# Kernel tuning notes

Measured on AMD Instinct MI355X. Metric: run time of the kernel, lower is better.

Reference implementation:

```python
import jax, jax.numpy as jnp
import numpy as np

B, T, I, H, NL, HORIZON, NQ = 256, 512, 64, 512, 2, 30, 3
MEDIAN_IDX = 1  # quantiles.index(0.5)


def _lstm_cell(xt, h, c, Wih, Whh, b):
    # PyTorch gate order: i, f, g, o
    g = xt @ Wih.T + h @ Whh.T + b
    i, f, gg, o = jnp.split(g, 4, axis=-1)
    c_new = jax.nn.sigmoid(f) * c + jax.nn.sigmoid(i) * jnp.tanh(gg)
    h_new = jax.nn.sigmoid(o) * jnp.tanh(c_new)
    return h_new, c_new


def _run_lstm_layer(xs, Wih, Whh, b):
    # xs: [T, B, in]; zero initial state (torch default)
    batch = xs.shape[1]
    hidden = Whh.shape[1]
    h0 = jnp.zeros((batch, hidden), xs.dtype)

    def step(carry, xt):
        h, c = carry
        h, c = _lstm_cell(xt, h, c, Wih, Whh, b)
        return (h, c), h

    (hT, cT), hs = jax.lax.scan(step, (h0, h0), xs)
    return hs, hT, cT


def setup_inputs() -> dict:
    key = jax.random.key(0)
    ks = jax.random.split(key, 24)
    k = 1.0 / np.sqrt(H)

    def u(kk, shape):
        return jax.random.uniform(kk, shape, jnp.float32, -k, k)

    inp = {
        "x": jax.random.normal(ks[0], (B, T, I), jnp.float32),
        # encoder layer 0 (input I) and layer 1 (input H)
        "enc_Wih0": u(ks[1], (4 * H, I)),
        "enc_Whh0": u(ks[2], (4 * H, H)),
        "enc_bih0": u(ks[3], (4 * H,)),
        "enc_bhh0": u(ks[4], (4 * H,)),
        "enc_Wih1": u(ks[5], (4 * H, H)),
        "enc_Whh1": u(ks[6], (4 * H, H)),
        "enc_bih1": u(ks[7], (4 * H,)),
        "enc_bhh1": u(ks[8], (4 * H,)),
        # decoder layer 0 (input H+1) and layer 1 (input H)
        "dec_Wih0": u(ks[9], (4 * H, H + 1)),
        "dec_Whh0": u(ks[10], (4 * H, H)),
        "dec_bih0": u(ks[11], (4 * H,)),
        "dec_bhh0": u(ks[12], (4 * H,)),
        "dec_Wih1": u(ks[13], (4 * H, H)),
        "dec_Whh1": u(ks[14], (4 * H, H)),
        "dec_bih1": u(ks[15], (4 * H,)),
        "dec_bhh1": u(ks[16], (4 * H,)),
        # attention: W [H,H] (no bias), V [H] (Linear(H,1) weight)
        "attn_W": u(ks[17], (H, H)),
        "attn_v": u(ks[18], (H,)),
        # output projection [NQ, H] + bias
        "out_W": u(ks[19], (NQ, H)),
        "out_b": u(ks[20], (NQ,)),
    }
    return inp


def reference(x, enc_Wih0, enc_Whh0, enc_bih0, enc_bhh0,
              enc_Wih1, enc_Whh1, enc_bih1, enc_bhh1,
              dec_Wih0, dec_Whh0, dec_bih0, dec_bhh0,
              dec_Wih1, dec_Whh1, dec_bih1, dec_bhh1,
              attn_W, attn_v, out_W, out_b):
    # ---- encoder: 2-layer LSTM over time (eval mode: no dropout) ----
    xs = jnp.transpose(x, (1, 0, 2))  # [T, B, I]
    hs0, _, _ = _run_lstm_layer(xs, enc_Wih0, enc_Whh0, enc_bih0 + enc_bhh0)
    hs1, h_last, c_last = _run_lstm_layer(hs0, enc_Wih1, enc_Whh1, enc_bih1 + enc_bhh1)
    encoder_outputs = jnp.transpose(hs1, (1, 0, 2))  # [B, T, H]

    # precompute W(encoder_outputs) once (same math as per-step recompute)
    enc_proj = jnp.einsum('bth,gh->btg', encoder_outputs, attn_W)  # [B, T, H]

    b_dec0 = dec_bih0 + dec_bhh0
    b_dec1 = dec_bih1 + dec_bhh1

    dec_input0 = x[:, -1, 0:1]  # [B, 1]

    def step(carry, _):
        h, c, inp = carry
        # Bahdanau attention
        dec_proj = h @ attn_W.T  # [B, H]
        energies = jnp.einsum('bth,h->bt', jnp.tanh(enc_proj + dec_proj[:, None, :]), attn_v)
        attn = jax.nn.softmax(energies, axis=1)  # [B, T]
        ctx = jnp.einsum('bt,bth->bh', attn, encoder_outputs)  # [B, H]
        # decoder LSTM, 1 timestep; both layers restart from the SAME (h, c)
        # (the module repeats the last layer's state across layers each step)
        x0 = jnp.concatenate([inp, ctx], axis=1)  # [B, H+1]
        h0, c0 = _lstm_cell(x0, h, c, dec_Wih0, dec_Whh0, b_dec0)
        h1, c1 = _lstm_cell(h0, h, c, dec_Wih1, dec_Whh1, b_dec1)
        out = h1 @ out_W.T + out_b  # [B, NQ]
        new_inp = out[:, MEDIAN_IDX:MEDIAN_IDX + 1]  # feed back median quantile
        return (h1, c1, new_inp), out

    _, preds = jax.lax.scan(step, (h_last, c_last, dec_input0), None, length=HORIZON)
    return jnp.transpose(preds, (1, 0, 2))  # [B, HORIZON, NQ]
```

## Files before the change

### kernel.cpp

```cpp
#include <hip/hip_runtime.h>


typedef _Float16 half_t;
typedef __attribute__((ext_vector_type(8)))  _Float16 f16x8;
typedef __attribute__((ext_vector_type(16))) float    f32x16;

#define MFMA(a,b,c) __builtin_amdgcn_mfma_f32_32x32x16_f16((a),(b),(c),0,0,0)
#define CBAR()      asm volatile("" ::: "memory")

template<int N> __device__ __forceinline__ void waitvm() {
  asm volatile("s_waitcnt vmcnt(%0)" :: "n"(N) : "memory");
}

__device__ __forceinline__ float fsig(float x)  { return 1.0f / (1.0f + __expf(-x)); }
__device__ __forceinline__ float ftanh(float x) { return 1.0f - 2.0f / (1.0f + __expf(2.0f * x)); }

union FU { float f; unsigned u; };
union HU { _Float16 h; unsigned short u; };

template<bool FAST>
__device__ __forceinline__ float ldfa(const float* p) {
  if constexpr (FAST) {
    float v;
    asm volatile("global_load_dword %0, %1, off sc0\n\ts_waitcnt vmcnt(0)"
                 : "=v"(v) : "v"(p) : "memory");
    return v;
  } else {
    unsigned v = __hip_atomic_load((const unsigned*)p, __ATOMIC_RELAXED, __HIP_MEMORY_SCOPE_AGENT);
    FU c; c.u = v; return c.f;
  }
}
template<bool FAST>
__device__ __forceinline__ void stfa(float* p, float v) {
  FU c; c.f = v;
  if constexpr (FAST)
    asm volatile("global_store_dword %0, %1, off sc0" :: "v"(p), "v"(c.u) : "memory");
  else
    __hip_atomic_store((unsigned*)p, c.u, __ATOMIC_RELAXED, __HIP_MEMORY_SCOPE_AGENT);
}
template<bool FAST>
__device__ __forceinline__ void stha(half_t* p, float v) {
  HU c; c.h = (half_t)v;
  if constexpr (FAST)
    asm volatile("global_store_short %0, %1, off sc0" :: "v"(p), "v"((unsigned)c.u) : "memory");
  else
    __hip_atomic_store((unsigned short*)p, c.u, __ATOMIC_RELAXED, __HIP_MEMORY_SCOPE_AGENT);
}
template<bool FAST>
__device__ __forceinline__ void st64(float* p, float a, float b) {
  FU x, y; x.f = a; y.f = b;
  unsigned long long v = (unsigned long long)x.u | ((unsigned long long)y.u << 32);
  if constexpr (FAST)
    asm volatile("global_store_dwordx2 %0, %1, off sc0" :: "v"(p), "v"(v) : "memory");
  else
    __hip_atomic_store((unsigned long long*)p, v, __ATOMIC_RELAXED, __HIP_MEMORY_SCOPE_AGENT);
}
template<bool FAST>
__device__ __forceinline__ void ld64(const float* p, float& a, float& b) {
  unsigned long long v;
  if constexpr (FAST) {
    asm volatile("global_load_dwordx2 %0, %1, off sc0\n\ts_waitcnt vmcnt(0)"
                 : "=v"(v) : "v"(p) : "memory");
  } else {
    v = __hip_atomic_load((const unsigned long long*)p, __ATOMIC_RELAXED, __HIP_MEMORY_SCOPE_AGENT);
  }
  FU x, y; x.u = (unsigned)v; y.u = (unsigned)(v >> 32); a = x.f; b = y.f;
}

static constexpr size_t O_X16 = 0;
static constexpr size_t O_WL0 = O_X16 + (size_t)512*256*128*2;
static constexpr size_t O_WL1 = O_WL0 + (size_t)2048*640*2;
static constexpr size_t O_WP1 = O_WL1 + (size_t)2048*1024*2;
static constexpr size_t O_WD0 = O_WP1 + (size_t)4672*512*2;
static constexpr size_t O_WD1 = O_WD0 + (size_t)2048*512*2;
static constexpr size_t O_BL0 = O_WD1 + (size_t)2048*512*2;
static constexpr size_t O_BL1 = O_BL0 + 8192;
static constexpr size_t O_BD0 = O_BL1 + 8192;
static constexpr size_t O_BD1 = O_BD0 + 8192;
static constexpr size_t O_W0C = O_BD1 + 8192;
static constexpr size_t O_H0B = O_W0C + 8192;
static constexpr size_t O_H1B = O_H0B + (size_t)2*256*512*2;
static constexpr size_t O_HD1 = O_H1B + (size_t)2*256*512*2;
static constexpr size_t O_H0D = O_HD1 + (size_t)256*512*2;
static constexpr size_t O_CTX = O_H0D + (size_t)256*512*2;
static constexpr size_t O_C0  = O_CTX + (size_t)256*512*2;
static constexpr size_t O_C1  = O_C0  + (size_t)256*512*4;
static constexpr size_t O_INP = O_C1  + (size_t)256*512*4;
static constexpr size_t O_GAT = O_INP + 1024;
static constexpr size_t O_EO  = O_GAT + (size_t)256*4672*4;
static constexpr size_t O_EP  = O_EO  + (size_t)256*512*512*2;
static constexpr size_t WS_NEED = O_EP + (size_t)256*512*512*2;

__device__ __align__(4096) unsigned char g_ws[WS_NEED];
__device__ int g_bar[2048];
__device__ int g_flags[1024];
__device__ int g_xcc[256];

#define WSH(o) ((half_t*)(g_ws + (o)))
#define WSCH(o) ((const half_t*)(g_ws + (o)))
#define WSF(o) ((float*)(g_ws + (o)))
#define WSCF(o) ((const float*)(g_ws + (o)))
#define BLINE(i) (g_bar + ((size_t)(i) << 5))

__device__ __forceinline__ int gperm(int n) { return (n & 3) * 512 + (n >> 2); }

__device__ __forceinline__ void gbarf(int g, int r, int step) {
  __syncthreads();
  if (threadIdx.x < 64) {
    if (threadIdx.x == 0)
      __hip_atomic_store(&g_flags[(g << 5) + r], step,
                         __ATOMIC_RELAXED, __HIP_MEMORY_SCOPE_AGENT);
    const int* fp = &g_flags[(g << 5) + (threadIdx.x & 31)];
    for (;;) {
      int v = __hip_atomic_load(fp, __ATOMIC_RELAXED, __HIP_MEMORY_SCOPE_AGENT);
      if (__all(v >= step)) break;
      __builtin_amdgcn_s_sleep(1);
    }
  }
  __syncthreads();
}

__device__ __forceinline__ void gbar_acq8() {
  __syncthreads();
  if (threadIdx.x == 0) {
    const int g = blockIdx.x & 7;
    int* cnt = BLINE(g);
    int* mst = BLINE(8);
    int* gs  = BLINE(16 + g);
    int old = __hip_atomic_load(gs, __ATOMIC_RELAXED, __HIP_MEMORY_SCOPE_AGENT);
    int a = __hip_atomic_fetch_add(cnt, 1, __ATOMIC_ACQ_REL, __HIP_MEMORY_SCOPE_AGENT);
    if (a == 31) {
      __hip_atomic_store(cnt, 0, __ATOMIC_RELAXED, __HIP_MEMORY_SCOPE_AGENT);
      int m = __hip_atomic_fetch_add(mst, 1, __ATOMIC_ACQ_REL, __HIP_MEMORY_SCOPE_AGENT);
      if (m == 7) {
        __hip_atomic_store(mst, 0, __ATOMIC_RELAXED, __HIP_MEMORY_SCOPE_AGENT);
        for (int q = 0; q < 8; q++)
          __hip_atomic_fetch_add(BLINE(16 + q), 1, __ATOMIC_RELEASE, __HIP_MEMORY_SCOPE_AGENT);
      }
    }
    while (__hip_atomic_load(gs, __ATOMIC_RELAXED, __HIP_MEMORY_SCOPE_AGENT) == old)
      __builtin_amdgcn_s_sleep(2);
    (void)__hip_atomic_load(gs, __ATOMIC_ACQUIRE, __HIP_MEMORY_SCOPE_AGENT);
  }
  __syncthreads();
}

template<int AX>
__device__ __forceinline__ void gld(const half_t* gp, char* lp) {
  __builtin_amdgcn_global_load_lds(
      (const __attribute__((address_space(1))) unsigned int*)gp,
      (__attribute__((address_space(3))) unsigned int*)lp, 16, 0, AX);
}

struct Seg { const half_t* p; int stride; int row0; };

template<int AXA, int AXB>
__device__ __forceinline__ void stageA(Seg sa, Seg sb, int cSplit, int c,
                                       int lane, int wid, char* dst) {
  bool isA = c < cSplit;
  Seg s = isA ? sa : sb;
  int kb = (isA ? c : (c - cSplit)) * 128;
  const half_t* gp = s.p + (size_t)(s.row0 + (lane & 31)) * s.stride
                         + kb + (wid << 4) + ((lane >> 5) << 3);
  if (isA) {
    gld<AXA>(gp, dst);
    gld<AXA>(gp + (size_t)32 * s.stride, dst + 1024);
  } else {
    gld<AXB>(gp, dst);
    gld<AXB>(gp + (size_t)32 * s.stride, dst + 1024);
  }
}

template<int C, int NC>
__device__ __forceinline__ void kks(int lane, int wid, char* asg, f32x16 acc[2][2],
                                    f16x8 (&b0)[4], f16x8 (&b1)[4]) {
  if constexpr (C < NC) {
    waitvm<4 * (NC - 1 - C)>();
    char* ab = asg + (size_t)(C * 8 + wid) * 2048 + lane * 16;
    f16x8 a0 = *(const f16x8*)ab;
    f16x8 a1 = *(const f16x8*)(ab + 1024);
    acc[0][0] = MFMA(a0, b0[C], acc[0][0]);
    acc[0][1] = MFMA(a0, b1[C], acc[0][1]);
    acc[1][0] = MFMA(a1, b0[C], acc[1][0]);
    acc[1][1] = MFMA(a1, b1[C], acc[1][1]);
    CBAR();
    kks<C + 1, NC>(lane, wid, asg, acc, b0, b1);
  }
}

template<int NC, int AXA, int AXB>
__device__ __forceinline__ void gemm_ks(Seg sa, Seg sb, int cSplit, const half_t* Wt,
                                        int lane, int wid, char* asg, f32x16 acc[2][2]) {
  const half_t* wb = Wt + (wid << 1) * 512 + lane * 8;
  f16x8 b0[4], b1[4];
  #pragma unroll
  for (int c = 0; c < NC; c++) {
    stageA<AXA, AXB>(sa, sb, cSplit, c, lane, wid, asg + (size_t)(c * 8 + wid) * 2048);
    CBAR();
    b0[c] = *(const f16x8*)(wb + (size_t)c * 8192);
    b1[c] = *(const f16x8*)(wb + (size_t)c * 8192 + 512);
    CBAR();
  }
  kks<0, NC>(lane, wid, asg, acc, b0, b1);
}

template<int C, int NC>
__device__ __forceinline__ void kks32(char* wslr, f32x16 (&acc)[2][2],
                                      f16x8 (&b0)[4], f16x8 (&b1)[4]) {
  if constexpr (C < NC) {
    waitvm<3 * (NC - 1 - C) + 2>();
    f16x8 a = *(const f16x8*)(wslr + C * 8192);
    acc[0][0] = MFMA(a, b0[C], acc[0][0]);
    acc[0][1] = MFMA(a, b1[C], acc[0][1]);
    CBAR();
    kks32<C + 1, NC>(wslr, acc, b0, b1);
  }
}

template<int NC, int AX>
__device__ __forceinline__ void gemm_ks32(const half_t* aP, const half_t* Wt,
                                          int lane, int wid, char* asg, f32x16 (&acc)[2][2]) {
  char* wsl = asg + wid * 1024;
  const half_t* wb = Wt + (wid << 1) * 512 + lane * 8;
  f16x8 b0[4], b1[4];
  #pragma unroll
  for (int c = 0; c < NC; c++) {
    gld<AX>(aP + c * 128, wsl + c * 8192);
    CBAR();
    b0[c] = *(const f16x8*)(wb + (size_t)c * 8192);
    b1[c] = *(const f16x8*)(wb + (size_t)c * 8192 + 512);
    CBAR();
  }
  kks32<0, NC>(wsl + lane * 16, acc, b0, b1);
}

template<int C>
__device__ __forceinline__ void encL0(const char* wslr, const f16x8 (&B0)[5],
                                      const f16x8 (&B1)[5], f32x16 (&acc)[2][2]) {
  if constexpr (C < 5) {
    waitvm<8 - C>();
    f16x8 a = *(const f16x8*)(wslr + C * 8192);
    acc[0][0] = MFMA(a, B0[C], acc[0][0]);
    acc[0][1] = MFMA(a, B1[C], acc[0][1]);
    CBAR();
    encL0<C + 1>(wslr, B0, B1, acc);
  }
}
template<int C>
__device__ __forceinline__ void encL1(const char* wslr, const f16x8 (&B0)[8],
                                      const f16x8 (&B1)[8], f32x16 (&acc)[2][2]) {
  if constexpr (C < 8) {
    if constexpr (C >= 4) waitvm<7 - C>();
    f16x8 a = *(const f16x8*)(wslr + (C + 1) * 8192);
    acc[1][0] = MFMA(a, B0[C], acc[1][0]);
    acc[1][1] = MFMA(a, B1[C], acc[1][1]);
    CBAR();
    encL1<C + 1>(wslr, B0, B1, acc);
  }
}

__device__ __forceinline__ void acc_wr(float* dst, int lane, f32x16 acc[2][2]) {
  #pragma unroll
  for (int t = 0; t < 4; t++) {
    f32x16 a = acc[t >> 1][t & 1];
    #pragma unroll
    for (int r4 = 0; r4 < 4; r4++)
      *(float4*)(dst + ((t * 4 + r4) * 64 + lane) * 4) =
          make_float4(a[r4*4], a[r4*4+1], a[r4*4+2], a[r4*4+3]);
  }
}
__device__ __forceinline__ void acc_add(const float* src, int lane, f32x16 acc[2][2]) {
  #pragma unroll
  for (int t = 0; t < 4; t++) {
    #pragma unroll
    for (int r4 = 0; r4 < 4; r4++) {
      float4 v = *(const float4*)(src + ((t * 4 + r4) * 64 + lane) * 4);
      acc[t>>1][t&1][r4*4]   += v.x;
      acc[t>>1][t&1][r4*4+1] += v.y;
      acc[t>>1][t&1][r4*4+2] += v.z;
      acc[t>>1][t&1][r4*4+3] += v.w;
    }
  }
}
__device__ __forceinline__ void reduce8(f32x16 acc[2][2], float* red, int lane, int wid) {
  if (wid >= 4) acc_wr(red + (size_t)(wid - 4) * 4096, lane, acc);
  __syncthreads();
  if (wid < 4) acc_add(red + (size_t)wid * 4096, lane, acc);
  if (wid == 2 || wid == 3) acc_wr(red + (size_t)wid * 4096, lane, acc);
  __syncthreads();
  if (wid < 2) {
    acc_add(red + (size_t)(wid + 2) * 4096, lane, acc);
    float* zone = red + 8192 + (size_t)wid * 4096;
    #pragma unroll
    for (int ms = 0; ms < 2; ms++)
      #pragma unroll
      for (int ns = 0; ns < 2; ns++)
        #pragma unroll
        for (int rr = 0; rr < 16; rr++) {
          int row = ms * 32 + (rr & 3) + ((rr >> 2) << 3) + ((lane >> 5) << 2);
          zone[row * 64 + ns * 32 + (lane & 31)] = acc[ms][ns][rr];
        }
  }
  __syncthreads();
}
__device__ __forceinline__ float4 rsum4(const float* red, int row, int col) {
  float4 a = *(const float4*)&red[8192 + row * 64 + col];
  float4 b = *(const float4*)&red[12288 + row * 64 + col];
  return make_float4(a.x + b.x, a.y + b.y, a.z + b.z, a.w + b.w);
}

template<bool FAST>
__device__ __noinline__ void run_all(int g, int r, const float* attn_v,
                                     const float* out_b, float* out,
                                     char* asg, float* red) {
  constexpr int AXH = FAST ? 1 : 17;
  constexpr size_t PP = (size_t)256 * 512;

  const half_t* x16 = WSCH(O_X16);
  const half_t* wL0 = WSCH(O_WL0);
  const half_t* wL1 = WSCH(O_WL1);
  const half_t* wP1 = WSCH(O_WP1);
  const half_t* wD0 = WSCH(O_WD0);
  const half_t* wD1 = WSCH(O_WD1);
  half_t* h0bB = WSH(O_H0B);
  half_t* h1bB = WSH(O_H1B);
  half_t* hd1  = WSH(O_HD1);
  half_t* h0d  = WSH(O_H0D);
  half_t* ctx  = WSH(O_CTX);
  half_t* eo   = WSH(O_EO);
  half_t* ep   = WSH(O_EP);
  float* c1 = WSF(O_C1);
  float* inp = WSF(O_INP);
  float* gates = WSF(O_GAT);

  const int tid = threadIdx.x;
  const int wid = tid >> 6;
  const int lane = tid & 63;
  const int m0 = g << 5;
  const f32x16 zv = {0,0,0,0,0,0,0,0,0,0,0,0,0,0,0,0};
  int bstep = 0;

  const int koff = (wid << 4) + ((lane >> 5) << 3);
  const size_t aofs = (size_t)(m0 + (lane & 31)) * 512 + koff;
  const size_t xofs = (size_t)(m0 + (lane & 31)) * 128 + koff;
  char* wsl = asg + wid * 1024;
  const char* wslr = wsl + lane * 16;

  {
    const int n0 = r << 6;
    const half_t* wb0 = wL0 + (size_t)r * (5 * 8192) + (wid << 1) * 512 + lane * 8;
    const half_t* wb1 = wL1 + (size_t)r * (8 * 8192) + (wid << 1) * 512 + lane * 8;
    f16x8 B0L0[5], B1L0[5], B0L1[8], B1L1[8];
    #pragma unroll
    for (int c = 0; c < 5; c++) {
      B0L0[c] = *(const f16x8*)(wb0 + (size_t)c * 8192);
      B1L0[c] = *(const f16x8*)(wb0 + (size_t)c * 8192 + 512);
    }
    #pragma unroll
    for (int c = 0; c < 8; c++) {
      B0L1[c] = *(const f16x8*)(wb1 + (size_t)c * 8192);
      B1L1[c] = *(const f16x8*)(wb1 + (size_t)c * 8192 + 512);
    }
    const int eu = tid & 15, ebl = tid >> 4;
    const float4 breg0 = *(const float4*)&(WSCF(O_BL0))[n0 + eu * 4];
    const float4 breg1 = *(const float4*)&(WSCF(O_BL1))[n0 + eu * 4];
    const int bg = m0 + ebl, ug = (r << 4) + eu;
    float creg0 = 0.f, creg1 = 0.f;

    for (int s = 0; s <= 512; s++) {
      {
        const int tc = s < 512 ? s : 511;
        const half_t* xp  = x16 + (((size_t)tc) << 15) + xofs;
        const half_t* h0p = h0bB + (size_t)((s + 1) & 1) * PP + aofs;
        const half_t* h1p = h1bB + (size_t)(s & 1) * PP + aofs;
        gld<0>(xp, wsl);
        #pragma unroll
        for (int c = 0; c < 4; c++) gld<AXH>(h0p + c * 128, wsl + (c + 1) * 8192);
        #pragma unroll
        for (int c = 0; c < 4; c++) gld<AXH>(h1p + c * 128, wsl + (c + 5) * 8192);
        CBAR();
      }
      f32x16 acc[2][2] = {{zv, zv}, {zv, zv}};
      encL0<0>(wslr, B0L0, B1L0, acc);
      encL1<0>(wslr, B0L1, B1L1, acc);
      reduce8(acc, red, lane, wid);
      if (s < 512) {
        float4 g4 = rsum4(red, ebl, eu * 4);
        float cn = fsig(g4.y + breg0.y) * creg0 + fsig(g4.x + breg0.x) * ftanh(g4.z + breg0.z);
        float hn = fsig(g4.w + breg0.w) * ftanh(cn);
        creg0 = cn;
        stha<FAST>(&h0bB[(size_t)(s & 1) * PP + (size_t)bg * 512 + ug], hn);
      }
      if (s > 0) {
        float4 g4 = rsum4(red, ebl + 32, eu * 4);
        float cn = fsig(g4.y + breg1.y) * creg1 + fsig(g4.x + breg1.x) * ftanh(g4.z + breg1.z);
        float hn = fsig(g4.w + breg1.w) * ftanh(cn);
        creg1 = cn;
        stha<FAST>(&h1bB[(size_t)((s + 1) & 1) * PP + (size_t)bg * 512 + ug], hn);
        eo[((size_t)bg * 512 + (s - 1)) * 512 + ug] = (half_t)hn;
      }
      gbarf(g, r, ++bstep);
    }
    c1[(size_t)bg * 512 + ug] = creg1;
  }
  gbar_acq8();

  for (int j = 0; j < 64; j++) {
    const int jj = (r << 6) + j;
    const int ml = jj >> 3;
    const int nt = jj & 7;
    const int row0 = (g << 14) + ml * 64;
    f32x16 acc[2][2] = {{zv, zv}, {zv, zv}};
    gemm_ks<4, 0, 0>(Seg{eo, 512, row0}, Seg{eo, 512, row0}, 4,
                     wP1 + (size_t)nt * (4 * 8192), lane, wid, asg, acc);
    reduce8(acc, red, lane, wid);
    {
      int row = tid >> 3, col = (tid & 7) * 8;
      float4 a0 = rsum4(red, row, col);
      float4 a1 = rsum4(red, row, col + 4);
      f16x8 h8;
      h8[0] = (half_t)a0.x; h8[1] = (half_t)a0.y; h8[2] = (half_t)a0.z; h8[3] = (half_t)a0.w;
      h8[4] = (half_t)a1.x; h8[5] = (half_t)a1.y; h8[6] = (half_t)a1.z; h8[7] = (half_t)a1.w;
      *(f16x8*)&ep[(size_t)(row0 + row) * 512 + nt * 64 + col] = h8;
    }
    __syncthreads();
  }
  gbar_acq8();

  for (int d = 0; d <= 30; d++) {
    const half_t* hs = (d == 0) ? (h1bB + PP) : hd1;

    for (int jj = r; jj < 73; jj += 32) {
      if (d == 30 && jj != 72) continue;
      f32x16 acc[2][2] = {{zv, zv}, {zv, zv}};
      gemm_ks32<4, AXH>(hs + aofs, wP1 + (size_t)jj * (4 * 8192), lane, wid, asg, acc);
      reduce8(acc, red, lane, wid);
      if (jj < 72) {
        int row = tid >> 4, col = (tid & 15) * 4;
        float4 v4 = rsum4(red, row, col);
        float* dst = &gates[(size_t)(m0 + row) * 4672 + jj * 64 + col];
        st64<FAST>(dst, v4.x, v4.y);
        st64<FAST>(dst + 2, v4.z, v4.w);
      } else if (d > 0) {
        if (tid < 32) {
          int bg = m0 + tid;
          float v0 = red[8192 + tid * 64 + 0] + red[12288 + tid * 64 + 0] + out_b[0];
          float v1 = red[8192 + tid * 64 + 1] + red[12288 + tid * 64 + 1] + out_b[1];
          float v2 = red[8192 + tid * 64 + 2] + red[12288 + tid * 64 + 2] + out_b[2];
          out[(size_t)bg * 90 + (d - 1) * 3 + 0] = v0;
          out[(size_t)bg * 90 + (d - 1) * 3 + 1] = v1;
          out[(size_t)bg * 90 + (d - 1) * 3 + 2] = v2;
          stfa<FAST>(&inp[bg], v1);
        }
      }
      __syncthreads();
    }
    gbarf(g, r, ++bstep);
    if (d == 30) break;

    {
      const int b = m0 + r;
      float* dpb = red;
      float* vb  = red + 512;
      float* eb  = red + 1024;
      float* ab2 = red + 2048;
      float* sc  = red + 2560;
      float* pm  = red + 4096;
      dpb[tid] = ldfa<FAST>(&gates[(size_t)b * 4672 + tid]);
      vb[tid]  = attn_v[tid];
      __syncthreads();
      float va[8], da[8];
      {
        float4 t0 = *(const float4*)&vb[lane * 8];
        float4 t1 = *(const float4*)&vb[lane * 8 + 4];
        float4 t2 = *(const float4*)&dpb[lane * 8];
        float4 t3 = *(const float4*)&dpb[lane * 8 + 4];
        va[0]=t0.x; va[1]=t0.y; va[2]=t0.z; va[3]=t0.w;
        va[4]=t1.x; va[5]=t1.y; va[6]=t1.z; va[7]=t1.w;
        da[0]=t2.x; da[1]=t2.y; da[2]=t2.z; da[3]=t2.w;
        da[4]=t3.x; da[5]=t3.y; da[6]=t3.z; da[7]=t3.w;
      }
      const half_t* eprow = ep + ((size_t)b << 18) + (size_t)(wid * 64) * 512 + lane * 8;
      for (int tt = 0; tt < 64; tt++) {
        f16x8 e8 = *(const f16x8*)(eprow + (size_t)tt * 512);
        float sum = 0.f;
        #pragma unroll
        for (int jq = 0; jq < 8; jq++)
          sum += va[jq] * ftanh((float)e8[jq] + da[jq]);
        #pragma unroll
        for (int off = 32; off > 0; off >>= 1) sum += __shfl_down(sum, off, 64);
        if (lane == 0) eb[wid * 64 + tt] = sum;
      }
      __syncthreads();
      float e0 = eb[tid];
      float mx = e0;
      #pragma unroll
      for (int off = 32; off > 0; off >>= 1) mx = fmaxf(mx, __shfl_xor(mx, off, 64));
      if (lane == 0) sc[wid] = mx;
      __syncthreads();
      mx = sc[0];
      #pragma unroll
      for (int q = 1; q < 8; q++) mx = fmaxf(mx, sc[q]);
      float x0 = __expf(e0 - mx);
      float ssum = x0;
      #pragma unroll
      for (int off = 32; off > 0; off >>= 1) ssum += __shfl_xor(ssum, off, 64);
      __syncthreads();
      if (lane == 0) sc[8 + wid] = ssum;
      __syncthreads();
      float tot = sc[8];
      #pragma unroll
      for (int q = 1; q < 8; q++) tot += sc[8 + q];
      float inv = 1.f / tot;
      ab2[tid] = x0 * inv;
      __syncthreads();
      float pacc[8] = {0,0,0,0,0,0,0,0};
      const half_t* eow = eo + ((size_t)b << 18) + (size_t)(wid * 64) * 512 + lane * 8;
      for (int tt = 0; tt < 64; tt++) {
        f16x8 h8 = *(const f16x8*)(eow + (size_t)tt * 512);
        float at = ab2[wid * 64 + tt];
        #pragma unroll
        for (int jq = 0; jq < 8; jq++) pacc[jq] += at * (float)h8[jq];
      }
      #pragma unroll
      for (int jq = 0; jq < 8; jq++) pm[wid * 512 + lane * 8 + jq] = pacc[jq];
      __syncthreads();
      float sctx = 0.f;
      #pragma unroll
      for (int w = 0; w < 8; w++) sctx += pm[w * 512 + tid];
      stha<FAST>(&ctx[((size_t)b << 9) + tid], sctx);
    }
    gbarf(g, r, ++bstep);

    {
      f32x16 acc[2][2] = {{zv, zv}, {zv, zv}};
      gemm_ks32<4, AXH>(ctx + aofs, wD0 + (size_t)r * (4 * 8192), lane, wid, asg, acc);
      reduce8(acc, red, lane, wid);
      const float* bD0 = WSCF(O_BD0);
      const float* w0c = WSCF(O_W0C);
      int u = tid & 15, bl = tid >> 4;
      int bg = m0 + bl, ug = (r << 4) + u, nl = (r << 6) + u * 4;
      float4 g4 = rsum4(red, bl, u * 4);
      float p0, p1, p2, p3;
      ld64<FAST>(&gates[(size_t)bg * 4672 + 512 + nl], p0, p1);
      ld64<FAST>(&gates[(size_t)bg * 4672 + 512 + nl + 2], p2, p3);
      float4 b4 = *(const float4*)&bD0[nl];
      float4 w4 = *(const float4*)&w0c[nl];
      float iv = ldfa<FAST>(&inp[bg]);
      float gi = g4.x + p0 + b4.x + iv * w4.x;
      float gf = g4.y + p1 + b4.y + iv * w4.y;
      float gz = g4.z + p2 + b4.z + iv * w4.z;
      float go = g4.w + p3 + b4.w + iv * w4.w;
      float cold = c1[(size_t)bg * 512 + ug];
      float cn = fsig(gf) * cold + fsig(gi) * ftanh(gz);
      stha<FAST>(&h0d[(size_t)bg * 512 + ug], fsig(go) * ftanh(cn));
    }
    gbarf(g, r, ++bstep);

    {
      f32x16 acc[2][2] = {{zv, zv}, {zv, zv}};
      gemm_ks32<4, AXH>(h0d + aofs, wD1 + (size_t)r * (4 * 8192), lane, wid, asg, acc);
      reduce8(acc, red, lane, wid);
      const float* bD1 = WSCF(O_BD1);
      int u = tid & 15, bl = tid >> 4;
      int bg = m0 + bl, ug = (r << 4) + u, nl = (r << 6) + u * 4;
      float4 g4 = rsum4(red, bl, u * 4);
      float p0, p1, p2, p3;
      ld64<FAST>(&gates[(size_t)bg * 4672 + 2560 + nl], p0, p1);
      ld64<FAST>(&gates[(size_t)bg * 4672 + 2560 + nl + 2], p2, p3);
      float4 b4 = *(const float4*)&bD1[nl];
      float gi = g4.x + p0 + b4.x;
      float gf = g4.y + p1 + b4.y;
      float gz = g4.z + p2 + b4.z;
      float go = g4.w + p3 + b4.w;
      float cold = c1[(size_t)bg * 512 + ug];
      float cn = fsig(gf) * cold + fsig(gi) * ftanh(gz);
      float hn = fsig(go) * ftanh(cn);
      c1[(size_t)bg * 512 + ug] = cn;
      stha<FAST>(&hd1[(size_t)bg * 512 + ug], hn);
    }
    gbarf(g, r, ++bstep);
  }
}

__global__ void __launch_bounds__(512, 2) kmain(const float* __restrict__ attn_v,
                                                const float* __restrict__ out_b,
                                                float* __restrict__ out) {
  __shared__ __align__(16) char asg[73728];
  __shared__ float red[16384];
  __shared__ int smode;

  const int g = blockIdx.x & 7;
  const int r = blockIdx.x >> 3;

  int xcc = 0;
  asm volatile("s_getreg_b32 %0, hwreg(HW_REG_XCC_ID)" : "=s"(xcc));
  if (threadIdx.x == 0)
    __hip_atomic_store(&g_xcc[blockIdx.x], xcc + 1,
                       __ATOMIC_RELAXED, __HIP_MEMORY_SCOPE_AGENT);
  gbar_acq8();
  if (threadIdx.x < 64) {
    int p = __hip_atomic_load(&g_xcc[((threadIdx.x & 31) << 3) | g],
                              __ATOMIC_RELAXED, __HIP_MEMORY_SCOPE_AGENT);
    int q = __hip_atomic_load(&g_xcc[((threadIdx.x & 31) << 3) | (g ^ 1)],
                              __ATOMIC_RELAXED, __HIP_MEMORY_SCOPE_AGENT);
    int p0 = __builtin_amdgcn_readfirstlane(p);
    int ok = (__all(p == p0) && !__all(q == p0)) ? 1 : 0;
    if (threadIdx.x == 0) smode = ok;
  }
  __syncthreads();
  if (smode) run_all<true>(g, r, attn_v, out_b, out, asg, red);
  else       run_all<false>(g, r, attn_v, out_b, out, asg, red);
}

__global__ void kpackB(size_t dstOff, int id, int Ntiles, int NC,
                       const float* s0, const float* s1,
                       const float* s2, const float* s3) {
  half_t* dst = (half_t*)(g_ws + dstOff);
  size_t total = (size_t)Ntiles * NC * 8192;
  size_t i = (size_t)blockIdx.x * 256 + threadIdx.x;
  size_t stride = (size_t)gridDim.x * 256;
  for (size_t e = i; e < total; e += stride) {
    int j = e & 7;
    int l = (e >> 3) & 63;
    int bh = (e >> 9) & 1;
    int w = (e >> 10) & 7;
    int tc = (int)(e >> 13);
    int c = tc % NC;
    int tile = tc / NC;
    int n = tile * 64 + bh * 32 + (l & 31);
    int k = c * 128 + w * 16 + ((l >> 5) << 3) + j;
    float v = 0.f;
    if (id == 0) {
      int pn = gperm(n);
      if (k < 64) v = s0[(size_t)pn * 64 + k];
      else if (k >= 128) v = s1[(size_t)pn * 512 + (k - 128)];
    } else if (id == 1) {
      int pn = gperm(n);
      v = (k < 512) ? s0[(size_t)pn * 512 + k] : s1[(size_t)pn * 512 + (k - 512)];
    } else if (id == 2) {
      if (n < 512) v = s0[((size_t)n << 9) + k];
      else if (n < 2560) v = s1[((size_t)gperm(n - 512) << 9) + k];
      else if (n < 4608) v = s2[((size_t)gperm(n - 2560) << 9) + k];
      else if (n < 4611) v = s3[((size_t)(n - 4608) << 9) + k];
    } else if (id == 3) {
      v = s0[(size_t)gperm(n) * 513 + 1 + k];
    } else {
      v = s0[((size_t)gperm(n) << 9) + k];
    }
    dst[e] = (half_t)v;
  }
}

__global__ void kmisc(const float* ebih0, const float* ebhh0, const float* ebih1, const float* ebhh1,
                      const float* dbih0, const float* dbhh0, const float* dbih1, const float* dbhh1,
                      const float* dWih0, const float* x) {
  float* bL0 = WSF(O_BL0);
  float* bL1 = WSF(O_BL1);
  float* bD0 = WSF(O_BD0);
  float* bD1 = WSF(O_BD1);
  float* w0c = WSF(O_W0C);
  half_t* h0b = WSH(O_H0B);
  half_t* h1b = WSH(O_H1B);
  float* c1 = WSF(O_C1);
  float* inp = WSF(O_INP);
  int i = blockIdx.x * 256 + threadIdx.x, stride = gridDim.x * 256;
  for (int idx = i; idx < 262144; idx += stride) {
    if (idx < 2048) {
      int pn = gperm(idx);
      bL0[idx] = ebih0[pn] + ebhh0[pn];
      bL1[idx] = ebih1[pn] + ebhh1[pn];
      bD0[idx] = dbih0[pn] + dbhh0[pn];
      bD1[idx] = dbih1[pn] + dbhh1[pn];
      w0c[idx] = dWih0[(size_t)pn * 513];
      g_bar[idx] = 0;
    }
    if (idx < 1024) g_flags[idx] = 0;
    if (idx < 256) { inp[idx] = x[((size_t)idx * 512 + 511) * 64]; g_xcc[idx] = 0; }
    h0b[idx] = (half_t)0.f;
    h1b[idx] = (half_t)0.f;
    if (idx < 131072) c1[idx] = 0.f;
  }
}

__global__ void kx16(const float* x) {
  half_t* dst = WSH(O_X16);
  size_t i = (size_t)blockIdx.x * 256 + threadIdx.x;
  size_t stride = (size_t)gridDim.x * 256;
  for (size_t e = i; e < (size_t)512 * 256 * 128; e += stride) {
    int t = (int)(e >> 15);
    int b = (int)((e >> 7) & 255);
    int ii = (int)(e & 127);
    dst[e] = (ii < 64) ? (half_t)x[((size_t)b * 512 + t) * 64 + ii] : (half_t)0.f;
  }
}

extern "C" void kernel_launch(void* const* d_in, const int* in_sizes, int n_in,
                              void* d_out, int out_size, void* d_ws, size_t ws_size,
                              hipStream_t stream) {
  const float* x     = (const float*)d_in[0];
  const float* eWih0 = (const float*)d_in[1];
  const float* eWhh0 = (const float*)d_in[2];
  const float* ebih0 = (const float*)d_in[3];
  const float* ebhh0 = (const float*)d_in[4];
  const float* eWih1 = (const float*)d_in[5];
  const float* eWhh1 = (const float*)d_in[6];
  const float* ebih1 = (const float*)d_in[7];
  const float* ebhh1 = (const float*)d_in[8];
  const float* dWih0 = (const float*)d_in[9];
  const float* dWhh0 = (const float*)d_in[10];
  const float* dbih0 = (const float*)d_in[11];
  const float* dbhh0 = (const float*)d_in[12];
  const float* dWih1 = (const float*)d_in[13];
  const float* dWhh1 = (const float*)d_in[14];
  const float* dbih1 = (const float*)d_in[15];
  const float* dbhh1 = (const float*)d_in[16];
  const float* attnW = (const float*)d_in[17];
  const float* attnv = (const float*)d_in[18];
  const float* outW  = (const float*)d_in[19];
  const float* outb  = (const float*)d_in[20];
  (void)in_sizes; (void)n_in; (void)out_size; (void)d_ws; (void)ws_size;

  kpackB<<<1024, 256, 0, stream>>>(O_WL0, 0, 32, 5, eWih0, eWhh0, nullptr, nullptr);
  kpackB<<<1024, 256, 0, stream>>>(O_WL1, 1, 32, 8, eWih1, eWhh1, nullptr, nullptr);
  kpackB<<<1024, 256, 0, stream>>>(O_WP1, 2, 73, 4, attnW, dWhh0, dWhh1, outW);
  kpackB<<<1024, 256, 0, stream>>>(O_WD0, 3, 32, 4, dWih0, nullptr, nullptr, nullptr);
  kpackB<<<1024, 256, 0, stream>>>(O_WD1, 4, 32, 4, dWih1, nullptr, nullptr, nullptr);
  kmisc<<<1024, 256, 0, stream>>>(ebih0, ebhh0, ebih1, ebhh1,
                                  dbih0, dbhh0, dbih1, dbhh1, dWih0, x);
  kx16<<<2048, 256, 0, stream>>>(x);

  float* outp = (float*)d_out;
  void* args[] = {(void*)&attnv, (void*)&outb, (void*)&outp};
  hipError_t e = hipLaunchCooperativeKernel((void*)kmain, dim3(256), dim3(512),
                                            args, 0, stream);
  if (e != hipSuccess) {
    kmain<<<dim3(256), dim3(512), 0, stream>>>(attnv, outb, outp);
  }
}
```

Baseline: 6.893 ms.

## Split persistent kernel into encoder, projection and decoder kernels with faster flag barriers

The single cooperative kernel is split into three launches: a persistent encoder recurrence, a separate full-grid encoder-projection GEMM with 2048 blocks, and a persistent decoder. The per-step encoder barrier now prefetches the next x tile before signalling and uses a lighter flag publish/poll (sc0 stores/loads, sleep only after several spins) in place of gbarf. This aims to cut per-step synchronisation latency in the 512-step recurrence and to give the projection GEMM better parallelism. The costs are extra launch overhead and an XCD vote per kernel, plus reliance on flag counters that continue across kernels (the decoder starts its step count at 1024).

```diff
diff --git a/kernel.cpp b/kernel.cpp
--- a/kernel.cpp
+++ b/kernel.cpp
@@ -104,18 +104,34 @@
 
 __device__ __forceinline__ int gperm(int n) { return (n & 3) * 512 + (n >> 2); }
 
+template<bool FAST>
+__device__ __forceinline__ void flag_pub(int* p, int v) {
+  __hip_atomic_store(p, v, __ATOMIC_RELAXED, __HIP_MEMORY_SCOPE_AGENT);
+  if constexpr (FAST)
+    asm volatile("global_store_dword %0, %1, off sc0" :: "v"(p), "v"(v) : "memory");
+}
+template<bool FAST>
+__device__ __forceinline__ void flag_poll(const int* fp, int step) {
+  int it = 0;
+  for (;;) {
+    int v;
+    ++it;
+    if (FAST && (it & 15) != 0) {
+      asm volatile("global_load_dword %0, %1, off sc0\n\ts_waitcnt vmcnt(0)"
+                   : "=v"(v) : "v"(fp) : "memory");
+    } else {
+      v = __hip_atomic_load(fp, __ATOMIC_RELAXED, __HIP_MEMORY_SCOPE_AGENT);
+    }
+    if (__all(v >= step)) break;
+    if (it > 6) __builtin_amdgcn_s_sleep(1);
+  }
+}
+template<bool FAST>
 __device__ __forceinline__ void gbarf(int g, int r, int step) {
   __syncthreads();
   if (threadIdx.x < 64) {
-    if (threadIdx.x == 0)
-      __hip_atomic_store(&g_flags[(g << 5) + r], step,
-                         __ATOMIC_RELAXED, __HIP_MEMORY_SCOPE_AGENT);
-    const int* fp = &g_flags[(g << 5) + (threadIdx.x & 31)];
-    for (;;) {
-      int v = __hip_atomic_load(fp, __ATOMIC_RELAXED, __HIP_MEMORY_SCOPE_AGENT);
-      if (__all(v >= step)) break;
-      __builtin_amdgcn_s_sleep(1);
-    }
+    if (threadIdx.x == 0) flag_pub<FAST>(&g_flags[(g << 5) + r], step);
+    flag_poll<FAST>(&g_flags[(g << 5) + (threadIdx.x & 31)], step);
   }
   __syncthreads();
 }
@@ -145,6 +161,27 @@
   __syncthreads();
 }
 
+__device__ __forceinline__ bool xcd_vote(int g) {
+  __shared__ int smode;
+  int xcc = 0;
+  asm volatile("s_getreg_b32 %0, hwreg(HW_REG_XCC_ID)" : "=s"(xcc));
+  if (threadIdx.x == 0)
+    __hip_atomic_store(&g_xcc[blockIdx.x], xcc + 1,
+                       __ATOMIC_RELAXED, __HIP_MEMORY_SCOPE_AGENT);
+  gbar_acq8();
+  if (threadIdx.x < 64) {
+    int p = __hip_atomic_load(&g_xcc[((threadIdx.x & 31) << 3) | g],
+                              __ATOMIC_RELAXED, __HIP_MEMORY_SCOPE_AGENT);
+    int q = __hip_atomic_load(&g_xcc[((threadIdx.x & 31) << 3) | (g ^ 1)],
+                              __ATOMIC_RELAXED, __HIP_MEMORY_SCOPE_AGENT);
+    int p0 = __builtin_amdgcn_readfirstlane(p);
+    int ok = (__all(p == p0) && !__all(q == p0)) ? 1 : 0;
+    if (threadIdx.x == 0) smode = ok;
+  }
+  __syncthreads();
+  return smode != 0;
+}
+
 template<int AX>
 __device__ __forceinline__ void gld(const half_t* gp, char* lp) {
   __builtin_amdgcn_global_load_lds(
@@ -154,54 +191,12 @@
 
 struct Seg { const half_t* p; int stride; int row0; };
 
-template<int AXA, int AXB>
-__device__ __forceinline__ void stageA(Seg sa, Seg sb, int cSplit, int c,
-                                       int lane, int wid, char* dst) {
-  bool isA = c < cSplit;
-  Seg s = isA ? sa : sb;
-  int kb = (isA ? c : (c - cSplit)) * 128;
+__device__ __forceinline__ void stageA64(Seg s, int c, int lane, int wid, char* dst) {
+  int kb = c * 128;
   const half_t* gp = s.p + (size_t)(s.row0 + (lane & 31)) * s.stride
                          + kb + (wid << 4) + ((lane >> 5) << 3);
-  if (isA) {
-    gld<AXA>(gp, dst);
-    gld<AXA>(gp + (size_t)32 * s.stride, dst + 1024);
-  } else {
-    gld<AXB>(gp, dst);
-    gld<AXB>(gp + (size_t)32 * s.stride, dst + 1024);
-  }
-}
-
-template<int C, int NC>
-__device__ __forceinline__ void kks(int lane, int wid, char* asg, f32x16 acc[2][2],
-                                    f16x8 (&b0)[4], f16x8 (&b1)[4]) {
-  if constexpr (C < NC) {
-    waitvm<4 * (NC - 1 - C)>();
-    char* ab = asg + (size_t)(C * 8 + wid) * 2048 + lane * 16;
-    f16x8 a0 = *(const f16x8*)ab;
-    f16x8 a1 = *(const f16x8*)(ab + 1024);
-    acc[0][0] = MFMA(a0, b0[C], acc[0][0]);
-    acc[0][1] = MFMA(a0, b1[C], acc[0][1]);
-    acc[1][0] = MFMA(a1, b0[C], acc[1][0]);
-    acc[1][1] = MFMA(a1, b1[C], acc[1][1]);
-    CBAR();
-    kks<C + 1, NC>(lane, wid, asg, acc, b0, b1);
-  }
-}
-
-template<int NC, int AXA, int AXB>
-__device__ __forceinline__ void gemm_ks(Seg sa, Seg sb, int cSplit, const half_t* Wt,
-                                        int lane, int wid, char* asg, f32x16 acc[2][2]) {
-  const half_t* wb = Wt + (wid << 1) * 512 + lane * 8;
-  f16x8 b0[4], b1[4];
-  #pragma unroll
-  for (int c = 0; c < NC; c++) {
-    stageA<AXA, AXB>(sa, sb, cSplit, c, lane, wid, asg + (size_t)(c * 8 + wid) * 2048);
-    CBAR();
-    b0[c] = *(const f16x8*)(wb + (size_t)c * 8192);
-    b1[c] = *(const f16x8*)(wb + (size_t)c * 8192 + 512);
-    CBAR();
-  }
-  kks<0, NC>(lane, wid, asg, acc, b0, b1);
+  gld<0>(gp, dst);
+  gld<0>(gp + (size_t)32 * s.stride, dst + 1024);
 }
 
 template<int C, int NC>
@@ -216,7 +211,6 @@
     kks32<C + 1, NC>(wslr, acc, b0, b1);
   }
 }
-
 template<int NC, int AX>
 __device__ __forceinline__ void gemm_ks32(const half_t* aP, const half_t* Wt,
                                           int lane, int wid, char* asg, f32x16 (&acc)[2][2]) {
@@ -310,35 +304,20 @@
 }
 
 template<bool FAST>
-__device__ __noinline__ void run_all(int g, int r, const float* attn_v,
-                                     const float* out_b, float* out,
-                                     char* asg, float* red) {
+__device__ __noinline__ void enc_body(int g, int r, char* asg, float* red) {
   constexpr int AXH = FAST ? 1 : 17;
   constexpr size_t PP = (size_t)256 * 512;
-
   const half_t* x16 = WSCH(O_X16);
-  const half_t* wL0 = WSCH(O_WL0);
-  const half_t* wL1 = WSCH(O_WL1);
-  const half_t* wP1 = WSCH(O_WP1);
-  const half_t* wD0 = WSCH(O_WD0);
-  const half_t* wD1 = WSCH(O_WD1);
   half_t* h0bB = WSH(O_H0B);
   half_t* h1bB = WSH(O_H1B);
-  half_t* hd1  = WSH(O_HD1);
-  half_t* h0d  = WSH(O_H0D);
-  half_t* ctx  = WSH(O_CTX);
   half_t* eo   = WSH(O_EO);
-  half_t* ep   = WSH(O_EP);
   float* c1 = WSF(O_C1);
-  float* inp = WSF(O_INP);
-  float* gates = WSF(O_GAT);
 
   const int tid = threadIdx.x;
   const int wid = tid >> 6;
   const int lane = tid & 63;
   const int m0 = g << 5;
   const f32x16 zv = {0,0,0,0,0,0,0,0,0,0,0,0,0,0,0,0};
-  int bstep = 0;
 
   const int koff = (wid << 4) + ((lane >> 5) << 3);
   const size_t aofs = (size_t)(m0 + (lane & 31)) * 512 + koff;
@@ -346,73 +325,111 @@
   char* wsl = asg + wid * 1024;
   const char* wslr = wsl + lane * 16;
 
-  {
-    const int n0 = r << 6;
-    const half_t* wb0 = wL0 + (size_t)r * (5 * 8192) + (wid << 1) * 512 + lane * 8;
-    const half_t* wb1 = wL1 + (size_t)r * (8 * 8192) + (wid << 1) * 512 + lane * 8;
-    f16x8 B0L0[5], B1L0[5], B0L1[8], B1L1[8];
+  const int n0 = r << 6;
+  const half_t* wb0 = WSCH(O_WL0) + (size_t)r * (5 * 8192) + (wid << 1) * 512 + lane * 8;
+  const half_t* wb1 = WSCH(O_WL1) + (size_t)r * (8 * 8192) + (wid << 1) * 512 + lane * 8;
+  f16x8 B0L0[5], B1L0[5], B0L1[8], B1L1[8];
+  #pragma unroll
+  for (int c = 0; c < 5; c++) {
+    B0L0[c] = *(const f16x8*)(wb0 + (size_t)c * 8192);
+    B1L0[c] = *(const f16x8*)(wb0 + (size_t)c * 8192 + 512);
+  }
+  #pragma unroll
+  for (int c = 0; c < 8; c++) {
+    B0L1[c] = *(const f16x8*)(wb1 + (size_t)c * 8192);
+    B1L1[c] = *(const f16x8*)(wb1 + (size_t)c * 8192 + 512);
+  }
+  const int eu = tid & 15, ebl = tid >> 4;
+  const float4 breg0 = *(const float4*)&(WSCF(O_BL0))[n0 + eu * 4];
+  const float4 breg1 = *(const float4*)&(WSCF(O_BL1))[n0 + eu * 4];
+  const int bg = m0 + ebl, ug = (r << 4) + eu;
+  float creg0 = 0.f, creg1 = 0.f;
+
+  gld<0>(x16 + xofs, wsl);
+
+  for (int s = 0; s <= 512; s++) {
+    {
+      const half_t* h0p = h0bB + (size_t)((s + 1) & 1) * PP + aofs;
+      const half_t* h1p = h1bB + (size_t)(s & 1) * PP + aofs;
+      #pragma unroll
+      for (int c = 0; c < 4; c++) gld<AXH>(h0p + c * 128, wsl + (c + 1) * 8192);
+      #pragma unroll
+      for (int c = 0; c < 4; c++) gld<AXH>(h1p + c * 128, wsl + (c + 5) * 8192);
+      CBAR();
+    }
+    f32x16 acc[2][2] = {{zv, zv}, {zv, zv}};
+    encL0<0>(wslr, B0L0, B1L0, acc);
+    encL1<0>(wslr, B0L1, B1L1, acc);
+    reduce8(acc, red, lane, wid);
+    if (s < 512) {
+      float4 g4 = rsum4(red, ebl, eu * 4);
+      float cn = fsig(g4.y + breg0.y) * creg0 + fsig(g4.x + breg0.x) * ftanh(g4.z + breg0.z);
+      float hn = fsig(g4.w + breg0.w) * ftanh(cn);
+      creg0 = cn;
+      stha<FAST>(&h0bB[(size_t)(s & 1) * PP + (size_t)bg * 512 + ug], hn);
+    }
+    if (s > 0) {
+      float4 g4 = rsum4(red, ebl + 32, eu * 4);
+      float cn = fsig(g4.y + breg1.y) * creg1 + fsig(g4.x + breg1.x) * ftanh(g4.z + breg1.z);
+      float hn = fsig(g4.w + breg1.w) * ftanh(cn);
+      creg1 = cn;
+      stha<FAST>(&h1bB[(size_t)((s + 1) & 1) * PP + (size_t)bg * 512 + ug], hn);
+      eo[((size_t)bg * 512 + (s - 1)) * 512 + ug] = (half_t)hn;
+    }
+    __syncthreads();
+    {
+      const int tc2 = (s < 511) ? (s + 1) : 511;
+      gld<0>(x16 + (((size_t)tc2) << 15) + xofs, wsl);
+    }
+    if (tid == 0) flag_pub<FAST>(&g_flags[(g << 5) + r], s + 1);
+    if (tid < 64) flag_poll<FAST>(&g_flags[(g << 5) + (tid & 31)], s + 1);
+    __builtin_amdgcn_s_barrier();
+  }
+  c1[(size_t)bg * 512 + ug] = creg1;
+}
+
+__global__ void __launch_bounds__(512, 2) kenc(int) {
+  __shared__ __align__(16) char asg[73728];
+  __shared__ float red[16384];
+  const int g = blockIdx.x & 7;
+  const int r = blockIdx.x >> 3;
+  if (xcd_vote(g)) enc_body<true>(g, r, asg, red);
+  else             enc_body<false>(g, r, asg, red);
+}
+
+__global__ void __launch_bounds__(512, 2) kproj(int) {
+  __shared__ __align__(16) char asg[65536];
+  __shared__ float red[16384];
+  const half_t* eo = WSCH(O_EO);
+  const half_t* wP1 = WSCH(O_WP1);
+  half_t* ep = WSH(O_EP);
+  const int tid = threadIdx.x;
+  const int wid = tid >> 6;
+  const int lane = tid & 63;
+  const f32x16 zv = {0,0,0,0,0,0,0,0,0,0,0,0,0,0,0,0};
+  const int row0 = blockIdx.x * 64;
+
+  #pragma unroll
+  for (int c = 0; c < 4; c++)
+    stageA64(Seg{eo, 512, row0}, c, lane, wid, asg + (size_t)(c * 8 + wid) * 2048);
+  waitvm<0>();
+  CBAR();
+
+  for (int nt = 0; nt < 8; nt++) {
+    const half_t* wb = wP1 + (size_t)nt * (4 * 8192) + (wid << 1) * 512 + lane * 8;
+    f32x16 acc[2][2] = {{zv, zv}, {zv, zv}};
     #pragma unroll
-    for (int c = 0; c < 5; c++) {
-      B0L0[c] = *(const f16x8*)(wb0 + (size_t)c * 8192);
-      B1L0[c] = *(const f16x8*)(wb0 + (size_t)c * 8192 + 512);
-    }
-    #pragma unroll
-    for (int c = 0; c < 8; c++) {
-      B0L1[c] = *(const f16x8*)(wb1 + (size_t)c * 8192);
-      B1L1[c] = *(const f16x8*)(wb1 + (size_t)c * 8192 + 512);
-    }
-    const int eu = tid & 15, ebl = tid >> 4;
-    const float4 breg0 = *(const float4*)&(WSCF(O_BL0))[n0 + eu * 4];
-    const float4 breg1 = *(const float4*)&(WSCF(O_BL1))[n0 + eu * 4];
-    const int bg = m0 + ebl, ug = (r << 4) + eu;
-    float creg0 = 0.f, creg1 = 0.f;
-
-    for (int s = 0; s <= 512; s++) {
-      {
-        const int tc = s < 512 ? s : 511;
-        const half_t* xp  = x16 + (((size_t)tc) << 15) + xofs;
-        const half_t* h0p = h0bB + (size_t)((s + 1) & 1) * PP + aofs;
-        const half_t* h1p = h1bB + (size_t)(s & 1) * PP + aofs;
-        gld<0>(xp, wsl);
-        #pragma unroll
-        for (int c = 0; c < 4; c++) gld<AXH>(h0p + c * 128, wsl + (c + 1) * 8192);
-        #pragma unroll
-        for (int c = 0; c < 4; c++) gld<AXH>(h1p + c * 128, wsl + (c + 5) * 8192);
-        CBAR();
-      }
-      f32x16 acc[2][2] = {{zv, zv}, {zv, zv}};
-      encL0<0>(wslr, B0L0, B1L0, acc);
-      encL1<0>(wslr, B0L1, B1L1, acc);
-      reduce8(acc, red, lane, wid);
-      if (s < 512) {
-        float4 g4 = rsum4(red, ebl, eu * 4);
-        float cn = fsig(g4.y + breg0.y) * creg0 + fsig(g4.x + breg0.x) * ftanh(g4.z + breg0.z);
-        float hn = fsig(g4.w + breg0.w) * ftanh(cn);
-        creg0 = cn;
-        stha<FAST>(&h0bB[(size_t)(s & 1) * PP + (size_t)bg * 512 + ug], hn);
-      }
-      if (s > 0) {
-        float4 g4 = rsum4(red, ebl + 32, eu * 4);
-        float cn = fsig(g4.y + breg1.y) * creg1 + fsig(g4.x + breg1.x) * ftanh(g4.z + breg1.z);
-        float hn = fsig(g4.w + breg1.w) * ftanh(cn);
-        creg1 = cn;
-        stha<FAST>(&h1bB[(size_t)((s + 1) & 1) * PP + (size_t)bg * 512 + ug], hn);
-        eo[((size_t)bg * 512 + (s - 1)) * 512 + ug] = (half_t)hn;
-      }
-      gbarf(g, r, ++bstep);
-    }
-    c1[(size_t)bg * 512 + ug] = creg1;
-  }
-  gbar_acq8();
-
-  for (int j = 0; j < 64; j++) {
-    const int jj = (r << 6) + j;
-    const int ml = jj >> 3;
-    const int nt = jj & 7;
-    const int row0 = (g << 14) + ml * 64;
-    f32x16 acc[2][2] = {{zv, zv}, {zv, zv}};
-    gemm_ks<4, 0, 0>(Seg{eo, 512, row0}, Seg{eo, 512, row0}, 4,
-                     wP1 + (size_t)nt * (4 * 8192), lane, wid, asg, acc);
+    for (int c = 0; c < 4; c++) {
+      f16x8 b0 = *(const f16x8*)(wb + (size_t)c * 8192);
+      f16x8 b1 = *(const f16x8*)(wb + (size_t)c * 8192 + 512);
+      const char* ab = asg + (size_t)(c * 8 + wid) * 2048 + lane * 16;
+      f16x8 a0 = *(const f16x8*)ab;
+      f16x8 a1 = *(const f16x8*)(ab + 1024);
+      acc[0][0] = MFMA(a0, b0, acc[0][0]);
+      acc[0][1] = MFMA(a0, b1, acc[0][1]);
+      acc[1][0] = MFMA(a1, b0, acc[1][0]);
+      acc[1][1] = MFMA(a1, b1, acc[1][1]);
+    }
     reduce8(acc, red, lane, wid);
     {
       int row = tid >> 3, col = (tid & 7) * 8;
@@ -425,7 +442,36 @@
     }
     __syncthreads();
   }
-  gbar_acq8();
+}
+
+template<bool FAST>
+__device__ __noinline__ void dec_body(int g, int r, const float* attn_v,
+                                      const float* out_b, float* out,
+                                      char* asg, float* red) {
+  constexpr int AXH = FAST ? 1 : 17;
+  constexpr size_t PP = (size_t)256 * 512;
+  const half_t* wP1 = WSCH(O_WP1);
+  const half_t* wD0 = WSCH(O_WD0);
+  const half_t* wD1 = WSCH(O_WD1);
+  half_t* h1bB = WSH(O_H1B);
+  half_t* hd1  = WSH(O_HD1);
+  half_t* h0d  = WSH(O_H0D);
+  half_t* ctx  = WSH(O_CTX);
+  const half_t* eo = WSCH(O_EO);
+  const half_t* ep = WSCH(O_EP);
+  float* c1 = WSF(O_C1);
+  float* inp = WSF(O_INP);
+  float* gates = WSF(O_GAT);
+
+  const int tid = threadIdx.x;
+  const int wid = tid >> 6;
+  const int lane = tid & 63;
+  const int m0 = g << 5;
+  const f32x16 zv = {0,0,0,0,0,0,0,0,0,0,0,0,0,0,0,0};
+  int bstep = 1024;
+
+  const int koff = (wid << 4) + ((lane >> 5) << 3);
+  const size_t aofs = (size_t)(m0 + (lane & 31)) * 512 + koff;
 
   for (int d = 0; d <= 30; d++) {
     const half_t* hs = (d == 0) ? (h1bB + PP) : hd1;
@@ -455,7 +501,7 @@
       }
       __syncthreads();
     }
-    gbarf(g, r, ++bstep);
+    gbarf<FAST>(g, r, ++bstep);
     if (d == 30) break;
 
     {
@@ -530,7 +576,7 @@
       for (int w = 0; w < 8; w++) sctx += pm[w * 512 + tid];
       stha<FAST>(&ctx[((size_t)b << 9) + tid], sctx);
     }
-    gbarf(g, r, ++bstep);
+    gbarf<FAST>(g, r, ++bstep);
 
     {
       f32x16 acc[2][2] = {{zv, zv}, {zv, zv}};
@@ -555,7 +601,7 @@
       float cn = fsig(gf) * cold + fsig(gi) * ftanh(gz);
       stha<FAST>(&h0d[(size_t)bg * 512 + ug], fsig(go) * ftanh(cn));
     }
-    gbarf(g, r, ++bstep);
+    gbarf<FAST>(g, r, ++bstep);
 
     {
       f32x16 acc[2][2] = {{zv, zv}, {zv, zv}};
@@ -579,38 +625,19 @@
       c1[(size_t)bg * 512 + ug] = cn;
       stha<FAST>(&hd1[(size_t)bg * 512 + ug], hn);
     }
-    gbarf(g, r, ++bstep);
-  }
-}
-
-__global__ void __launch_bounds__(512, 2) kmain(const float* __restrict__ attn_v,
-                                                const float* __restrict__ out_b,
-                                                float* __restrict__ out) {
-  __shared__ __align__(16) char asg[73728];
+    gbarf<FAST>(g, r, ++bstep);
+  }
+}
+
+__global__ void __launch_bounds__(512, 2) kdec(const float* __restrict__ attn_v,
+                                               const float* __restrict__ out_b,
+                                               float* __restrict__ out) {
+  __shared__ __align__(16) char asg[32768];
   __shared__ float red[16384];
-  __shared__ int smode;
-
   const int g = blockIdx.x & 7;
   const int r = blockIdx.x >> 3;
-
-  int xcc = 0;
-  asm volatile("s_getreg_b32 %0, hwreg(HW_REG_XCC_ID)" : "=s"(xcc));
-  if (threadIdx.x == 0)
-    __hip_atomic_store(&g_xcc[blockIdx.x], xcc + 1,
-                       __ATOMIC_RELAXED, __HIP_MEMORY_SCOPE_AGENT);
-  gbar_acq8();
-  if (threadIdx.x < 64) {
-    int p = __hip_atomic_load(&g_xcc[((threadIdx.x & 31) << 3) | g],
-                              __ATOMIC_RELAXED, __HIP_MEMORY_SCOPE_AGENT);
-    int q = __hip_atomic_load(&g_xcc[((threadIdx.x & 31) << 3) | (g ^ 1)],
-                              __ATOMIC_RELAXED, __HIP_MEMORY_SCOPE_AGENT);
-    int p0 = __builtin_amdgcn_readfirstlane(p);
-    int ok = (__all(p == p0) && !__all(q == p0)) ? 1 : 0;
-    if (threadIdx.x == 0) smode = ok;
-  }
-  __syncthreads();
-  if (smode) run_all<true>(g, r, attn_v, out_b, out, asg, red);
-  else       run_all<false>(g, r, attn_v, out_b, out, asg, red);
+  if (xcd_vote(g)) dec_body<true>(g, r, attn_v, out_b, out, asg, red);
+  else             dec_body<false>(g, r, attn_v, out_b, out, asg, red);
 }
 
 __global__ void kpackB(size_t dstOff, int id, int Ntiles, int NC,
@@ -730,11 +757,17 @@
                                   dbih0, dbhh0, dbih1, dbhh1, dWih0, x);
   kx16<<<2048, 256, 0, stream>>>(x);
 
+  int zero = 0;
+  void* eargs[] = {(void*)&zero};
+  hipError_t e1 = hipLaunchCooperativeKernel((void*)kenc, dim3(256), dim3(512),
+                                             eargs, 0, stream);
+  if (e1 != hipSuccess) kenc<<<dim3(256), dim3(512), 0, stream>>>(0);
+
+  kproj<<<dim3(2048), dim3(512), 0, stream>>>(0);
+
   float* outp = (float*)d_out;
-  void* args[] = {(void*)&attnv, (void*)&outb, (void*)&outp};
-  hipError_t e = hipLaunchCooperativeKernel((void*)kmain, dim3(256), dim3(512),
-                                            args, 0, stream);
-  if (e != hipSuccess) {
-    kmain<<<dim3(256), dim3(512), 0, stream>>>(attnv, outb, outp);
-  }
-}
+  void* dargs[] = {(void*)&attnv, (void*)&outb, (void*)&outp};
+  hipError_t e2 = hipLaunchCooperativeKernel((void*)kdec, dim3(256), dim3(512),
+                                             dargs, 0, stream);
+  if (e2 != hipSuccess) kdec<<<dim3(256), dim3(512), 0, stream>>>(attnv, outb, outp);
+}
```

After: 10.25 ms. 48.7% more time.
